# Optimization experiments

Hardware: AMD Instinct MI355X
Metric: run time of the kernel (lower is better)

## Reference

```python
import jax, jax.numpy as jnp
import numpy as np

B, Cin, H, W = 4, 256, 96, 96
CC = 64      # corr_channels
K = 5        # corr_kernel_size
OC = 32      # out_channels
PAD = K // 2 # pad='k' with odd K -> symmetric pad 2


def setup_inputs() -> dict:
    key = jax.random.key(0)
    k0, k1, k2, k3, k4 = jax.random.split(key, 5)
    x = jax.random.normal(k0, (B, Cin, H, W), jnp.float32)
    extract_w = jax.random.normal(k1, (CC, Cin, 3, 3), jnp.float32) * 0.02
    extract_b = jax.random.normal(k2, (CC,), jnp.float32) * 0.02
    reg_w = jax.random.normal(k3, (OC, CC, K, K), jnp.float32) * 0.02
    reg_b = jax.random.normal(k4, (OC,), jnp.float32) * 0.02
    return {"x": x, "extract_w": extract_w, "extract_b": extract_b,
            "reg_w": reg_w, "reg_b": reg_b}


def reference(x, extract_w, extract_b, reg_w, reg_b):
    # extract_input: 3x3 conv, padding 1 (NCHW / OIHW)
    f = jax.lax.conv_general_dilated(
        x, extract_w, window_strides=(1, 1), padding=[(1, 1), (1, 1)],
        dimension_numbers=("NCHW", "OIHW", "NCHW"))
    f = f + extract_b[None, :, None, None]  # [B, CC, H, W]

    # LocalAutoCorr2D: per-channel product of each center feature with its
    # KxK neighborhood (pad='k', stride=1 -> corr grid == feature grid).
    xp = jnp.pad(f, ((0, 0), (0, 0), (PAD, PAD), (PAD, PAD)))
    nh, nw = H, W
    # patches[b,c,u,v,i,j] = xp[b,c,i+u,j+v]; static KxK loop, vectorized over B/C/HW
    patches = jnp.stack(
        [jnp.stack([xp[:, :, u:u + nh, v:v + nw] for v in range(K)], axis=2)
         for u in range(K)], axis=2)               # [B, CC, K, K, nh, nw]
    center = patches[:, :, K // 2, K // 2]         # [B, CC, nh, nw]
    corr = patches * center[:, :, None, None]      # [B, CC, K, K, nh, nw]

    # full contraction over (c,u,v) for every corr-grid location.
    y = jnp.einsum("bcuvij,ocuv->boij", corr, reg_w) + reg_b[None, :, None, None]
    # permute=True -> [B, OC, nh, nw]
    return y
```

## Files before the change

kernel.cpp:

```cpp
#include <hip/hip_runtime.h>
#include <hip/hip_bf16.h>

#define BATCH 4
#define CIN 256
#define H 96
#define W 96
#define CC 64
#define OC 32

typedef __attribute__((ext_vector_type(8))) short bf16x8;
typedef __attribute__((ext_vector_type(4))) float f32x4;
typedef __attribute__((ext_vector_type(4))) unsigned short u16x4;
typedef __attribute__((ext_vector_type(4))) unsigned int u32x4;

#define XT_OFF  0
#define WT_OFF  19668992
#define RWT_OFF 19963904
#define FT_OFF  20066304

__device__ inline unsigned short f2bf(float v) {
    __hip_bfloat16 t = __float2bfloat16(v);
    return *reinterpret_cast<unsigned short*>(&t);
}
__device__ inline float bf2f(short b) {
    return __uint_as_float(((unsigned int)(unsigned short)b) << 16);
}

__device__ inline void gload_lds16(const __hip_bfloat16* g, void* l) {
    __builtin_amdgcn_global_load_lds(
        (const __attribute__((address_space(1))) unsigned int*)g,
        (__attribute__((address_space(3))) unsigned int*)l, 16, 0, 0);
}

__global__ __launch_bounds__(256) void prep_xt_kernel(
    const float* __restrict__ x, const float* __restrict__ ew,
    const float* __restrict__ rw, __hip_bfloat16* __restrict__ xt,
    __hip_bfloat16* __restrict__ wt, __hip_bfloat16* __restrict__ rwt,
    __hip_bfloat16* __restrict__ ft)
{
    const int bid = blockIdx.x;
    const int tid = threadIdx.x;

    if (bid >= 392) {
        const int pb = bid - 392;
        if (pb < 576) {
            int idx = pb * 256 + tid;
            int e   = idx & 7;
            int m   = (idx >> 3) & 15;
            int cb  = (idx >> 7) & 31;
            int ccg = (idx >> 12) & 3;
            int k   = idx >> 14;
            int cc = ccg * 16 + m, ci = cb * 8 + e;
            wt[idx] = __float2bfloat16(ew[(cc * CIN + ci) * 9 + k]);
        } else if (pb < 776) {
            int idx = (pb - 576) * 256 + tid;
            if (idx >= 50 * 2 * 64 * 8) return;
            int e    = idx & 7;
            int lane = (idx >> 3) & 63;
            int mt   = (idx >> 9) & 1;
            int kc   = idx >> 10;
            int g = lane >> 4, m = lane & 15;
            int o  = mt * 16 + m;
            int k  = kc * 32 + g * 8 + e;
            int uv = k >> 6, c = k & 63;
            rwt[idx] = __float2bfloat16(rw[(o * CC + c) * 25 + uv]);
        } else {
            int idx = (pb - 776) * 256 + tid;
            if (idx >= 4 * 6272) return;
            int b = idx / 6272, t = idx % 6272;
            int q = t & 7, pid = t >> 3;
            int r, c;
            if (pid < 400) {
                int rr = pid / 100;
                r = (rr < 2) ? rr : rr + 96;
                c = pid % 100;
            } else {
                int p2 = pid - 400;
                r = 2 + (p2 >> 2);
                int c2 = p2 & 3;
                c = (c2 < 2) ? c2 : c2 + 96;
            }
            *(u32x4*)(ft + ((size_t)((b * 100 + r) * 100 + c)) * 64 + q * 8) = (u32x4){0u,0u,0u,0u};
        }
        return;
    }

    const int r = bid % 98;
    const int b = bid / 98;
    __hip_bfloat16* rowp = xt + ((size_t)(b * 98 + r)) * 98 * 256;
    const int gi = r - 1;

    if (gi < 0 || gi >= H) {
        u32x4* p = (u32x4*)rowp;
        const u32x4 z = (u32x4){0u,0u,0u,0u};
        for (int t = tid; t < 98 * 256 * 2 / 16; t += 256) p[t] = z;
        return;
    }

    __shared__ __align__(16) __hip_bfloat16 lds[96][264];

    for (int cich = 0; cich < 8; ++cich) {
        int ci = cich * 32 + (tid >> 3);
        const float* src = x + ((size_t)((b * CIN + ci) * H + gi)) * W;
        for (int coli = 0; coli < 3; ++coli) {
            int col = coli * 32 + (tid & 7) * 4;
            float4 v = *(const float4*)(src + col);
            lds[col + 0][ci] = __float2bfloat16(v.x);
            lds[col + 1][ci] = __float2bfloat16(v.y);
            lds[col + 2][ci] = __float2bfloat16(v.z);
            lds[col + 3][ci] = __float2bfloat16(v.w);
        }
    }
    __syncthreads();

    u32x4* dst16 = (u32x4*)rowp;
#pragma unroll
    for (int it = 0; it < 12; ++it) {
        int u = it * 256 + tid;
        int col = u >> 5, ci8 = u & 31;
        u32x4 v = *(const u32x4*)&lds[col][ci8 * 8];
        dst16[(col + 1) * 32 + ci8] = v;
    }
    if (tid < 32) dst16[tid] = (u32x4){0u,0u,0u,0u};
    else if (tid < 64) dst16[97 * 32 + (tid - 32)] = (u32x4){0u,0u,0u,0u};
}

__global__ __launch_bounds__(256) void conv_mfma4_kernel(
    const __hip_bfloat16* __restrict__ xt, const __hip_bfloat16* __restrict__ wt,
    const float* __restrict__ eb, __hip_bfloat16* __restrict__ ft)
{
    const int bid = blockIdx.x;
    const int job = (bid & 7) * 72 + (bid >> 3);
    const int jb = job % 3;
    const int iq = (job / 3) % 24;
    const int zz = job / 72;
    const int b = zz >> 1, ch = zz & 1;
    const int j0 = jb * 32, i0 = iq * 4;
    const int tid = threadIdx.x;
    const int wid = tid >> 6;
    const int lane = tid & 63;
    const int g = lane >> 4, m = lane & 15;

    __shared__ __align__(16) char bbuf[2][14336];

    const int start = (wid < 2) ? wid * 256 : 512 + (wid - 2) * 192;
    const int nslot = (wid < 2) ? 4 : 3;

    const __hip_bfloat16* src0; const __hip_bfloat16* src1;
    const __hip_bfloat16* src2; const __hip_bfloat16* src3;
    int dst0, dst1, dst2, dst3;
#define SLOT_INIT(J, SRC, DST)                                                  \
    {                                                                           \
        int U = start + (J) * 64 + lane;                                        \
        if (U > 863) U = 863;                                                   \
        int s = U & 3, pxr = U >> 2;                                            \
        int px = pxr % 36, r = pxr / 36;                                        \
        int q = s ^ ((px >> 1) & 3);                                            \
        SRC = xt + ((size_t)((b * 98 + i0 + r) * 98 + j0 + px)) * 256 + q * 8;  \
        DST = (start + (J) * 64) * 16;                                          \
    }
    SLOT_INIT(0, src0, dst0)
    SLOT_INIT(1, src1, dst1)
    SLOT_INIT(2, src2, dst2)
    SLOT_INIT(3, src3, dst3)
#undef SLOT_INIT

#define STAGE(T, NB)                                                            \
    {                                                                           \
        const int co = (T) * 32;                                                \
        char* lb = &bbuf[(NB)][0];                                              \
        gload_lds16(src0 + co, lb + dst0);                                      \
        gload_lds16(src1 + co, lb + dst1);                                      \
        gload_lds16(src2 + co, lb + dst2);                                      \
        if (nslot > 3) gload_lds16(src3 + co, lb + dst3);                       \
    }

    STAGE(0, 0)
    __syncthreads();

    f32x4 acc00 = (f32x4){0.f,0.f,0.f,0.f}, acc01 = (f32x4){0.f,0.f,0.f,0.f};
    f32x4 acc10 = (f32x4){0.f,0.f,0.f,0.f}, acc11 = (f32x4){0.f,0.f,0.f,0.f};

    const __hip_bfloat16* wA = wt + (ch * 2) * 4096 + g * 128 + m * 8;

    for (int t = 0; t < 8; ++t) {
        if (t < 7) STAGE(t + 1, (t + 1) & 1)

        const char* bb = &bbuf[t & 1][0];
        const __hip_bfloat16* wa = wA + t * 512;
#pragma unroll
        for (int ku = 0; ku < 3; ++ku) {
#pragma unroll
            for (int kv = 0; kv < 3; ++kv) {
                const int k = ku * 3 + kv;
                bf16x8 a0 = *(const bf16x8*)(wa + k * 16384);
                bf16x8 a1 = *(const bf16x8*)(wa + k * 16384 + 4096);
                const int r = wid + ku;
                const int px0 = m + kv, px1 = px0 + 16;
                bf16x8 b0 = *(const bf16x8*)(bb + ((r * 36 + px0) * 4 + (g ^ ((px0 >> 1) & 3))) * 16);
                bf16x8 b1 = *(const bf16x8*)(bb + ((r * 36 + px1) * 4 + (g ^ ((px1 >> 1) & 3))) * 16);
                acc00 = __builtin_amdgcn_mfma_f32_16x16x32_bf16(a0, b0, acc00, 0, 0, 0);
                acc01 = __builtin_amdgcn_mfma_f32_16x16x32_bf16(a0, b1, acc01, 0, 0, 0);
                acc10 = __builtin_amdgcn_mfma_f32_16x16x32_bf16(a1, b0, acc10, 0, 0, 0);
                acc11 = __builtin_amdgcn_mfma_f32_16x16x32_bf16(a1, b1, acc11, 0, 0, 0);
            }
        }
        __syncthreads();
    }
#undef STAGE

    __hip_bfloat16* out = ft + ((size_t)((b * 100 + i0 + wid + 2) * 100 + (j0 + 2))) * 64;
#pragma unroll
    for (int mt = 0; mt < 2; ++mt) {
        const int ccb = (ch * 2 + mt) * 16 + g * 4;
        float bias[4];
#pragma unroll
        for (int r = 0; r < 4; ++r) bias[r] = eb[ccb + r];
        f32x4 aN0 = (mt == 0) ? acc00 : acc10;
        f32x4 aN1 = (mt == 0) ? acc01 : acc11;
        u16x4 p0, p1;
#pragma unroll
        for (int r = 0; r < 4; ++r) {
            p0[r] = f2bf(aN0[r] + bias[r]);
            p1[r] = f2bf(aN1[r] + bias[r]);
        }
        *(u16x4*)(out + (0 * 16 + m) * 64 + ccb) = p0;
        *(u16x4*)(out + (1 * 16 + m) * 64 + ccb) = p1;
    }
}

__global__ __launch_bounds__(256) void corrproj_mfma2_kernel(
    const __hip_bfloat16* __restrict__ ft, const __hip_bfloat16* __restrict__ rwt,
    const float* __restrict__ rb, float* __restrict__ y)
{
    const int bid = blockIdx.x;
    const int job = (bid & 7) * 72 + (bid >> 3);
    const int jb = job % 3;
    const int iy = (job / 3) % 48;
    const int b  = job / 144;
    const int jc0 = jb * 32, i0 = iy * 2;
    const int tid = threadIdx.x;
    const int wave = tid >> 6, lane = tid & 63;
    const int g = lane >> 4, m = lane & 15;
    const int rw = wave >> 1, pw = wave & 1;

    __shared__ __align__(16) char wnd[6 * 36 * 128];
    __shared__ __align__(16) char asub[2][5 * 2 * 1024];

    {
        const __hip_bfloat16* base = ft + ((size_t)((b * 100 + i0) * 100 + jc0)) * 64;
#pragma unroll
        for (int it = 0; it < 7; ++it) {
            int u = it * 256 + tid;
            if (u < 1728) {
                int q = u & 7, rc = u >> 3;
                int col = rc % 36, r = rc / 36;
                u32x4 v = *(const u32x4*)(base + ((size_t)(r * 100 + col)) * 64 + q * 8);
                *(u32x4*)(wnd + (r * 36 + col) * 128 + ((q ^ (col & 7)) << 4)) = v;
            }
        }
    }
    {
        const u32x4* src = (const u32x4*)rwt;
        u32x4* dst = (u32x4*)&asub[0][0];
        dst[tid] = src[tid];
        dst[tid + 256] = src[tid + 256];
        if (tid < 128) dst[tid + 512] = src[tid + 512];
    }
    __syncthreads();

    float cen[16];
    {
        const int colc = pw * 16 + m + 2;
        const char* cb = wnd + ((rw + 2) * 36 + colc) * 128;
        bf16x8 c0 = *(const bf16x8*)(cb + ((g ^ (colc & 7)) << 4));
        bf16x8 c1 = *(const bf16x8*)(cb + (((4 + g) ^ (colc & 7)) << 4));
#pragma unroll
        for (int e = 0; e < 8; ++e) {
            cen[e]     = bf2f(c0[e]);
            cen[8 + e] = bf2f(c1[e]);
        }
    }

    f32x4 acc0 = (f32x4){0.f, 0.f, 0.f, 0.f};
    f32x4 acc1 = (f32x4){0.f, 0.f, 0.f, 0.f};

    for (int sc = 0; sc < 10; ++sc) {
        u32x4 p0, p1, p2;
        const bool pf = (sc < 9);
        if (pf) {
            const u32x4* src = (const u32x4*)rwt + (sc + 1) * 640;
            p0 = src[tid];
            p1 = src[tid + 256];
            if (tid < 128) p2 = src[tid + 512];
        }

        const char* ab = &asub[sc & 1][0];
#pragma unroll
        for (int kk = 0; kk < 5; ++kk) {
            const int kc = sc * 5 + kk;
            const int uv = kc >> 1, h = kc & 1;
            const int u = uv / 5, v = uv - u * 5;
            bf16x8 a0 = *(const bf16x8*)(ab + (kk * 2 + 0) * 1024 + lane * 16);
            bf16x8 a1 = *(const bf16x8*)(ab + (kk * 2 + 1) * 1024 + lane * 16);
            const int col = pw * 16 + m + v;
            const char* sb = wnd + ((rw + u) * 36 + col) * 128;
            bf16x8 s = *(const bf16x8*)(sb + (((h * 4 + g) ^ (col & 7)) << 4));
            bf16x8 hb;
#pragma unroll
            for (int e = 0; e < 8; ++e)
                hb[e] = (short)f2bf(bf2f(s[e]) * cen[h * 8 + e]);
            acc0 = __builtin_amdgcn_mfma_f32_16x16x32_bf16(a0, hb, acc0, 0, 0, 0);
            acc1 = __builtin_amdgcn_mfma_f32_16x16x32_bf16(a1, hb, acc1, 0, 0, 0);
        }

        if (pf) {
            u32x4* dst = (u32x4*)&asub[(sc + 1) & 1][0];
            dst[tid] = p0;
            dst[tid + 256] = p1;
            if (tid < 128) dst[tid + 512] = p2;
        }
        __syncthreads();
    }

    const int i = i0 + rw, j0 = jc0 + pw * 16;
#pragma unroll
    for (int r = 0; r < 4; ++r) {
        int o0 = g * 4 + r;
        y[((size_t)(b * OC + o0) * H + i) * W + j0 + m] = acc0[r] + rb[o0];
        int o1 = 16 + g * 4 + r;
        y[((size_t)(b * OC + o1) * H + i) * W + j0 + m] = acc1[r] + rb[o1];
    }
}

extern "C" void kernel_launch(void* const* d_in, const int* in_sizes, int n_in,
                              void* d_out, int out_size, void* d_ws, size_t ws_size,
                              hipStream_t stream) {
    const float* x  = (const float*)d_in[0];
    const float* ew = (const float*)d_in[1];
    const float* eb = (const float*)d_in[2];
    const float* rw = (const float*)d_in[3];
    const float* rb = (const float*)d_in[4];
    float* y = (float*)d_out;

    char* ws = (char*)d_ws;
    __hip_bfloat16* xt  = (__hip_bfloat16*)(ws + XT_OFF);
    __hip_bfloat16* wt  = (__hip_bfloat16*)(ws + WT_OFF);
    __hip_bfloat16* rwt = (__hip_bfloat16*)(ws + RWT_OFF);
    __hip_bfloat16* ft  = (__hip_bfloat16*)(ws + FT_OFF);

    prep_xt_kernel<<<1266, 256, 0, stream>>>(x, ew, rw, xt, wt, rwt, ft);
    conv_mfma4_kernel<<<576, 256, 0, stream>>>(xt, wt, eb, ft);
    corrproj_mfma2_kernel<<<576, 256, 0, stream>>>(ft, rwt, rb, y);
}
```

Measured before the change: 54.22 us.

## Fuse fp32-to-bf16 input transpose into conv kernel, drop padded xt buffer

Removes the prep pass that converted x to a padded channel-last bf16 tensor in workspace. The conv kernel now reads fp32 x directly with per-thread gathered scalar loads, masks the halo, converts to bf16 and writes into the swizzled LDS tile, with loads issued before the MFMA loop and LDS writes after it. This avoids a full extra write and read of the roughly 19 MB transposed input. The cost is 27 uncoalesced-ish scalar global loads per thread per chunk, extra registers, and re-reading overlapping halo data across blocks.

```diff
diff --git a/kernel.cpp b/kernel.cpp
--- a/kernel.cpp
+++ b/kernel.cpp
@@ -13,10 +13,9 @@
 typedef __attribute__((ext_vector_type(4))) unsigned short u16x4;
 typedef __attribute__((ext_vector_type(4))) unsigned int u32x4;
 
-#define XT_OFF  0
-#define WT_OFF  19668992
-#define RWT_OFF 19963904
-#define FT_OFF  20066304
+#define WT_OFF  0
+#define RWT_OFF 294912
+#define FT_OFF  397312
 
 __device__ inline unsigned short f2bf(float v) {
     __hip_bfloat16 t = __float2bfloat16(v);
@@ -26,107 +25,56 @@
     return __uint_as_float(((unsigned int)(unsigned short)b) << 16);
 }
 
-__device__ inline void gload_lds16(const __hip_bfloat16* g, void* l) {
-    __builtin_amdgcn_global_load_lds(
-        (const __attribute__((address_space(1))) unsigned int*)g,
-        (__attribute__((address_space(3))) unsigned int*)l, 16, 0, 0);
-}
-
-__global__ __launch_bounds__(256) void prep_xt_kernel(
-    const float* __restrict__ x, const float* __restrict__ ew,
-    const float* __restrict__ rw, __hip_bfloat16* __restrict__ xt,
+__global__ __launch_bounds__(256) void prep_small_kernel(
+    const float* __restrict__ ew, const float* __restrict__ rw,
     __hip_bfloat16* __restrict__ wt, __hip_bfloat16* __restrict__ rwt,
     __hip_bfloat16* __restrict__ ft)
 {
-    const int bid = blockIdx.x;
+    const int pb = blockIdx.x;
     const int tid = threadIdx.x;
-
-    if (bid >= 392) {
-        const int pb = bid - 392;
-        if (pb < 576) {
-            int idx = pb * 256 + tid;
-            int e   = idx & 7;
-            int m   = (idx >> 3) & 15;
-            int cb  = (idx >> 7) & 31;
-            int ccg = (idx >> 12) & 3;
-            int k   = idx >> 14;
-            int cc = ccg * 16 + m, ci = cb * 8 + e;
-            wt[idx] = __float2bfloat16(ew[(cc * CIN + ci) * 9 + k]);
-        } else if (pb < 776) {
-            int idx = (pb - 576) * 256 + tid;
-            if (idx >= 50 * 2 * 64 * 8) return;
-            int e    = idx & 7;
-            int lane = (idx >> 3) & 63;
-            int mt   = (idx >> 9) & 1;
-            int kc   = idx >> 10;
-            int g = lane >> 4, m = lane & 15;
-            int o  = mt * 16 + m;
-            int k  = kc * 32 + g * 8 + e;
-            int uv = k >> 6, c = k & 63;
-            rwt[idx] = __float2bfloat16(rw[(o * CC + c) * 25 + uv]);
+    if (pb < 576) {
+        int idx = pb * 256 + tid;
+        int e   = idx & 7;
+        int m   = (idx >> 3) & 15;
+        int cb  = (idx >> 7) & 31;
+        int ccg = (idx >> 12) & 3;
+        int k   = idx >> 14;
+        int cc = ccg * 16 + m, ci = cb * 8 + e;
+        wt[idx] = __float2bfloat16(ew[(cc * CIN + ci) * 9 + k]);
+    } else if (pb < 776) {
+        int idx = (pb - 576) * 256 + tid;
+        if (idx >= 50 * 2 * 64 * 8) return;
+        int e    = idx & 7;
+        int lane = (idx >> 3) & 63;
+        int mt   = (idx >> 9) & 1;
+        int kc   = idx >> 10;
+        int g = lane >> 4, m = lane & 15;
+        int o  = mt * 16 + m;
+        int k  = kc * 32 + g * 8 + e;
+        int uv = k >> 6, c = k & 63;
+        rwt[idx] = __float2bfloat16(rw[(o * CC + c) * 25 + uv]);
+    } else {
+        int idx = (pb - 776) * 256 + tid;
+        if (idx >= 4 * 6272) return;
+        int b = idx / 6272, t = idx % 6272;
+        int q = t & 7, pid = t >> 3;
+        int r, c;
+        if (pid < 400) {
+            int rr = pid / 100;
+            r = (rr < 2) ? rr : rr + 96;
+            c = pid % 100;
         } else {
-            int idx = (pb - 776) * 256 + tid;
-            if (idx >= 4 * 6272) return;
-            int b = idx / 6272, t = idx % 6272;
-            int q = t & 7, pid = t >> 3;
-            int r, c;
-            if (pid < 400) {
-                int rr = pid / 100;
-                r = (rr < 2) ? rr : rr + 96;
-                c = pid % 100;
-            } else {
-                int p2 = pid - 400;
-                r = 2 + (p2 >> 2);
-                int c2 = p2 & 3;
-                c = (c2 < 2) ? c2 : c2 + 96;
-            }
-            *(u32x4*)(ft + ((size_t)((b * 100 + r) * 100 + c)) * 64 + q * 8) = (u32x4){0u,0u,0u,0u};
-        }
-        return;
-    }
-
-    const int r = bid % 98;
-    const int b = bid / 98;
-    __hip_bfloat16* rowp = xt + ((size_t)(b * 98 + r)) * 98 * 256;
-    const int gi = r - 1;
-
-    if (gi < 0 || gi >= H) {
-        u32x4* p = (u32x4*)rowp;
-        const u32x4 z = (u32x4){0u,0u,0u,0u};
-        for (int t = tid; t < 98 * 256 * 2 / 16; t += 256) p[t] = z;
-        return;
-    }
-
-    __shared__ __align__(16) __hip_bfloat16 lds[96][264];
-
-    for (int cich = 0; cich < 8; ++cich) {
-        int ci = cich * 32 + (tid >> 3);
-        const float* src = x + ((size_t)((b * CIN + ci) * H + gi)) * W;
-        for (int coli = 0; coli < 3; ++coli) {
-            int col = coli * 32 + (tid & 7) * 4;
-            float4 v = *(const float4*)(src + col);
-            lds[col + 0][ci] = __float2bfloat16(v.x);
-            lds[col + 1][ci] = __float2bfloat16(v.y);
-            lds[col + 2][ci] = __float2bfloat16(v.z);
-            lds[col + 3][ci] = __float2bfloat16(v.w);
-        }
-    }
-    __syncthreads();
-
-    u32x4* dst16 = (u32x4*)rowp;
-#pragma unroll
-    for (int it = 0; it < 12; ++it) {
-        int u = it * 256 + tid;
-        int col = u >> 5, ci8 = u & 31;
-        u32x4 v = *(const u32x4*)&lds[col][ci8 * 8];
-        dst16[(col + 1) * 32 + ci8] = v;
-    }
-    if (tid < 32) dst16[tid] = (u32x4){0u,0u,0u,0u};
-    else if (tid < 64) dst16[97 * 32 + (tid - 32)] = (u32x4){0u,0u,0u,0u};
-}
-
-__global__ __launch_bounds__(256) void conv_mfma4_kernel(
-    const __hip_bfloat16* __restrict__ xt, const __hip_bfloat16* __restrict__ wt,
+            int p2 = pid - 400;
+            r = 2 + (p2 >> 2);
+            int c2 = p2 & 3;
+            c = (c2 < 2) ? c2 : c2 + 96;
+        }
+        *(u32x4*)(ft + ((size_t)((b * 100 + r) * 100 + c)) * 64 + q * 8) = (u32x4){0u,0u,0u,0u};
+    }
+}
+
+__global__ __launch_bounds__(256) void conv_mfma5_kernel(
+    const float* __restrict__ x, const __hip_bfloat16* __restrict__ wt,
     const float* __restrict__ eb, __hip_bfloat16* __restrict__ ft)
 {
     const int bid = blockIdx.x;
@@ -141,41 +89,45 @@
     const int lane = tid & 63;
     const int g = lane >> 4, m = lane & 15;
 
-    __shared__ __align__(16) char bbuf[2][14336];
-
-    const int start = (wid < 2) ? wid * 256 : 512 + (wid - 2) * 192;
-    const int nslot = (wid < 2) ? 4 : 3;
-
-    const __hip_bfloat16* src0; const __hip_bfloat16* src1;
-    const __hip_bfloat16* src2; const __hip_bfloat16* src3;
-    int dst0, dst1, dst2, dst3;
-#define SLOT_INIT(J, SRC, DST)                                                  \
+    __shared__ __align__(16) char bbuf[2][13824];
+
+    int goff[27];
+    int loff[27];
+    unsigned mask = 0;
+    {
+        int e = tid;
+#pragma unroll
+        for (int i = 0; i < 27; ++i, e += 256) {
+            int rc = e / 36, col = e - rc * 36;
+            int r = rc >> 5, ci = rc & 31;
+            int gi = i0 - 1 + r;
+            int gj = j0 - 1 + col;
+            bool ok = ((unsigned)gi < 96u) && ((unsigned)gj < 96u);
+            int gic = ok ? gi : 0;
+            int gjc = ok ? gj : 0;
+            goff[i] = ((b * CIN + ci) * H + gic) * W + gjc;
+            if (ok) mask |= (1u << i);
+            loff[i] = ((r * 36 + col) * 4 + ((ci >> 3) ^ ((col >> 1) & 3))) * 16 + (ci & 7) * 2;
+        }
+    }
+
+    float v[27];
+#define LOADC(T)                                                                \
     {                                                                           \
-        int U = start + (J) * 64 + lane;                                        \
-        if (U > 863) U = 863;                                                   \
-        int s = U & 3, pxr = U >> 2;                                            \
-        int px = pxr % 36, r = pxr / 36;                                        \
-        int q = s ^ ((px >> 1) & 3);                                            \
-        SRC = xt + ((size_t)((b * 98 + i0 + r) * 98 + j0 + px)) * 256 + q * 8;  \
-        DST = (start + (J) * 64) * 16;                                          \
-    }
-    SLOT_INIT(0, src0, dst0)
-    SLOT_INIT(1, src1, dst1)
-    SLOT_INIT(2, src2, dst2)
-    SLOT_INIT(3, src3, dst3)
-#undef SLOT_INIT
-
-#define STAGE(T, NB)                                                            \
+        const float* xp = x + (size_t)(T) * 32 * (H * W);                       \
+        _Pragma("unroll") for (int i = 0; i < 27; ++i) v[i] = xp[goff[i]];      \
+    }
+#define WRITEC(NB)                                                              \
     {                                                                           \
-        const int co = (T) * 32;                                                \
         char* lb = &bbuf[(NB)][0];                                              \
-        gload_lds16(src0 + co, lb + dst0);                                      \
-        gload_lds16(src1 + co, lb + dst1);                                      \
-        gload_lds16(src2 + co, lb + dst2);                                      \
-        if (nslot > 3) gload_lds16(src3 + co, lb + dst3);                       \
-    }
-
-    STAGE(0, 0)
+        _Pragma("unroll") for (int i = 0; i < 27; ++i) {                        \
+            float f = ((mask >> i) & 1u) ? v[i] : 0.f;                          \
+            *(unsigned short*)(lb + loff[i]) = f2bf(f);                         \
+        }                                                                       \
+    }
+
+    LOADC(0)
+    WRITEC(0)
     __syncthreads();
 
     f32x4 acc00 = (f32x4){0.f,0.f,0.f,0.f}, acc01 = (f32x4){0.f,0.f,0.f,0.f};
@@ -184,7 +136,7 @@
     const __hip_bfloat16* wA = wt + (ch * 2) * 4096 + g * 128 + m * 8;
 
     for (int t = 0; t < 8; ++t) {
-        if (t < 7) STAGE(t + 1, (t + 1) & 1)
+        if (t < 7) LOADC(t + 1)
 
         const char* bb = &bbuf[t & 1][0];
         const __hip_bfloat16* wa = wA + t * 512;
@@ -205,9 +157,12 @@
                 acc11 = __builtin_amdgcn_mfma_f32_16x16x32_bf16(a1, b1, acc11, 0, 0, 0);
             }
         }
+
+        if (t < 7) WRITEC((t + 1) & 1)
         __syncthreads();
     }
-#undef STAGE
+#undef LOADC
+#undef WRITEC
 
     __hip_bfloat16* out = ft + ((size_t)((b * 100 + i0 + wid + 2) * 100 + (j0 + 2))) * 64;
 #pragma unroll
@@ -344,12 +299,11 @@
     float* y = (float*)d_out;
 
     char* ws = (char*)d_ws;
-    __hip_bfloat16* xt  = (__hip_bfloat16*)(ws + XT_OFF);
     __hip_bfloat16* wt  = (__hip_bfloat16*)(ws + WT_OFF);
     __hip_bfloat16* rwt = (__hip_bfloat16*)(ws + RWT_OFF);
     __hip_bfloat16* ft  = (__hip_bfloat16*)(ws + FT_OFF);
 
-    prep_xt_kernel<<<1266, 256, 0, stream>>>(x, ew, rw, xt, wt, rwt, ft);
-    conv_mfma4_kernel<<<576, 256, 0, stream>>>(xt, wt, eb, ft);
+    prep_small_kernel<<<874, 256, 0, stream>>>(ew, rw, wt, rwt, ft);
+    conv_mfma5_kernel<<<576, 256, 0, stream>>>(x, wt, eb, ft);
     corrproj_mfma2_kernel<<<576, 256, 0, stream>>>(ft, rwt, rb, y);
 }
```

Result: slower. 63.87 us (+17.8%).
